# Optimization experiments

Hardware: AMD Instinct MI355X
Metric: run time of the kernel (lower is better)

The kernel has to match this reference:

```python
import jax, jax.numpy as jnp
import numpy as np

B, T, HID = 2, 2048, 1024
NH, HD = 16, 64          # attn_heads, head_size (NH*HD == HID)
FF = 4 * HID
LN_EPS = 1e-5            # torch nn.LayerNorm default


def setup_inputs() -> dict:
    key = jax.random.key(0)
    ks = jax.random.split(key, 14)
    s = lambda fan_in: fan_in ** -0.5
    return {
        "embedding": jax.random.normal(ks[0], (B, T, HID), jnp.float32),
        # per-head q/k/v projections stacked: [HID, NH, HD] (no bias, as in torch code)
        "Wq": jax.random.normal(ks[1], (HID, NH, HD), jnp.float32) * s(HID),
        "Wk": jax.random.normal(ks[2], (HID, NH, HD), jnp.float32) * s(HID),
        "Wv": jax.random.normal(ks[3], (HID, NH, HD), jnp.float32) * s(HID),
        "Wo": jax.random.normal(ks[4], (HID, HID), jnp.float32) * s(HID),
        "W1": jax.random.normal(ks[5], (HID, FF), jnp.float32) * s(HID),
        "b1": jnp.zeros((FF,), jnp.float32),
        "W2": jax.random.normal(ks[6], (FF, HID), jnp.float32) * s(FF),
        "b2": jnp.zeros((HID,), jnp.float32),
        "g1": jnp.ones((HID,), jnp.float32),
        "be1": jnp.zeros((HID,), jnp.float32),
        "g2": jnp.ones((HID,), jnp.float32),
        "be2": jnp.zeros((HID,), jnp.float32),
    }


def _layer_norm(h, g, b):
    mu = jnp.mean(h, axis=-1, keepdims=True)
    var = jnp.mean(jnp.square(h - mu), axis=-1, keepdims=True)
    return (h - mu) * jax.lax.rsqrt(var + LN_EPS) * g + b


def _block(x, Wq, Wk, Wv, Wo, W1, b1, W2, b2, g1, be1, g2, be2):
    # --- causal multi-head self-attention (pre-LN) ---
    h = _layer_norm(x, g1, be1)
    q = jnp.einsum('btd,dhk->bhtk', h, Wq)
    k = jnp.einsum('btd,dhk->bhtk', h, Wk)
    v = jnp.einsum('btd,dhk->bhtk', h, Wv)
    scores = jnp.einsum('bhtk,bhsk->bhts', q, k) * (HD ** -0.5)
    causal = jnp.tril(jnp.ones((T, T), bool))
    scores = jnp.where(causal, scores, -jnp.inf)
    attn = jax.nn.softmax(scores, axis=-1)
    ctx = jnp.einsum('bhts,bhsk->bhtk', attn, v)          # [B,NH,T,HD]
    ctx = ctx.transpose(0, 2, 1, 3).reshape(x.shape[0], x.shape[1], HID)
    x = x + ctx @ Wo
    # --- feed-forward (pre-LN) ---
    h2 = _layer_norm(x, g2, be2)
    ff = jax.nn.relu(h2 @ W1 + b1) @ W2 + b2
    return x + ff


def reference(embedding, Wq, Wk, Wv, Wo, W1, b1, W2, b2, g1, be1, g2, be2):
    return _block(embedding, Wq, Wk, Wv, Wo, W1, b1, W2, b2, g1, be1, g2, be2)
```

## Files before the change

kernel.cpp:

```cpp
#include <hip/hip_runtime.h>
#include <math.h>

#define HIDDEN 1024
#define SEQ    2048
#define NHEAD  16
#define HDIM   64
#define ROWS   (2 * SEQ)

typedef float  floatx4  __attribute__((ext_vector_type(4)));
typedef float  floatx16 __attribute__((ext_vector_type(16)));
typedef __bf16 bf16x8   __attribute__((ext_vector_type(8)));
typedef __bf16 bf16x4   __attribute__((ext_vector_type(4)));

#define AS1(p) ((const __attribute__((address_space(1))) void*)(p))
#define AS3(p) ((__attribute__((address_space(3))) void*)(p))

#define SWZ(row, chunk) ((((chunk) ^ ((row) & 7)) * 8))

__global__ __launch_bounds__(256) void prep_all(const float* __restrict__ Wq,
                                                const float* __restrict__ Wk,
                                                const float* __restrict__ Wv,
                                                const float* __restrict__ Wo,
                                                const float* __restrict__ W1,
                                                const float* __restrict__ W2,
                                                __bf16* __restrict__ BtQKV,
                                                __bf16* __restrict__ BtO,
                                                __bf16* __restrict__ Bt1,
                                                __bf16* __restrict__ Bt2,
                                                const float* __restrict__ emb,
                                                const float* __restrict__ g1,
                                                const float* __restrict__ be1,
                                                __bf16* __restrict__ h,
                                                float* __restrict__ xout) {
    int id = blockIdx.x;
    int tid = threadIdx.x;
    if (id >= 12288) {
        int row = id - 12288;
        size_t i = (size_t)row * HIDDEN + tid * 4;
        float4 v = *(const float4*)(emb + i);
        *(float4*)(xout + i) = v;
        float s  = v.x + v.y + v.z + v.w;
        float s2 = v.x * v.x + v.y * v.y + v.z * v.z + v.w * v.w;
#pragma unroll
        for (int off = 1; off < 64; off <<= 1) {
            s  += __shfl_xor(s, off, 64);
            s2 += __shfl_xor(s2, off, 64);
        }
        __shared__ float red[8];
        int wid = tid >> 6;
        if ((tid & 63) == 0) { red[wid] = s; red[wid + 4] = s2; }
        __syncthreads();
        s  = red[0] + red[1] + red[2] + red[3];
        s2 = red[4] + red[5] + red[6] + red[7];
        float mu  = s * (1.0f / HIDDEN);
        float var = fmaxf(s2 * (1.0f / HIDDEN) - mu * mu, 0.0f);
        float inv = rsqrtf(var + 1e-5f);
        float4 gv = *(const float4*)(g1 + tid * 4);
        float4 bv = *(const float4*)(be1 + tid * 4);
        bf16x4 o;
        o[0] = (__bf16)((v.x - mu) * inv * gv.x + bv.x);
        o[1] = (__bf16)((v.y - mu) * inv * gv.y + bv.y);
        o[2] = (__bf16)((v.z - mu) * inv * gv.z + bv.z);
        o[3] = (__bf16)((v.w - mu) * inv * gv.w + bv.w);
        *(bf16x4*)(h + i) = o;
        return;
    }
    __shared__ float t[32][33];
    const float* in; __bf16* out; int K, N, nt, kt;
    if (id < 4096) {
        int job = id >> 10, tt = id & 1023;
        nt = tt & 31; kt = tt >> 5; K = 1024; N = 1024;
        if (job == 0)      { in = Wq; out = BtQKV; }
        else if (job == 1) { in = Wk; out = BtQKV + 1024 * 1024; }
        else if (job == 2) { in = Wv; out = BtQKV + 2 * 1024 * 1024; }
        else               { in = Wo; out = BtO; }
    } else if (id < 8192) {
        int tt = id - 4096;
        nt = tt & 127; kt = tt >> 7; K = 1024; N = 4096; in = W1; out = Bt1;
    } else {
        int tt = id - 8192;
        nt = tt & 31; kt = tt >> 5; K = 4096; N = 1024; in = W2; out = Bt2;
    }
    int n0 = nt * 32, k0 = kt * 32;
    int r  = tid >> 3;
    int c4 = (tid & 7) * 4;
    float4 v = *(const float4*)(in + (size_t)(k0 + r) * N + n0 + c4);
    t[r][c4 + 0] = v.x; t[r][c4 + 1] = v.y; t[r][c4 + 2] = v.z; t[r][c4 + 3] = v.w;
    __syncthreads();
    bf16x4 o;
    o[0] = (__bf16)t[c4 + 0][r];
    o[1] = (__bf16)t[c4 + 1][r];
    o[2] = (__bf16)t[c4 + 2][r];
    o[3] = (__bf16)t[c4 + 3][r];
    int n = n0 + r, k = k0 + c4;
    size_t blk = (size_t)(n >> 5) * (K >> 4) + (k >> 4);
    int ln = ((k >> 3) & 1) * 32 + (n & 31);
    *(bf16x4*)(out + blk * 512 + ln * 8 + (k & 7)) = o;
}

__global__ __launch_bounds__(256) void red_ln(const float* __restrict__ b2,
                                              const float* __restrict__ g,
                                              const float* __restrict__ beta,
                                              float* __restrict__ out,
                                              __bf16* __restrict__ h2) {
    int row = blockIdx.x;
    int tid = threadIdx.x;
    size_t i = (size_t)row * HIDDEN + tid * 4;
    float4 v = *(const float4*)(out + i);
    float s  = v.x + v.y + v.z + v.w;
    float s2 = v.x * v.x + v.y * v.y + v.z * v.z + v.w * v.w;
#pragma unroll
    for (int off = 1; off < 64; off <<= 1) {
        s  += __shfl_xor(s, off, 64);
        s2 += __shfl_xor(s2, off, 64);
    }
    __shared__ float red[8];
    int wid = tid >> 6;
    if ((tid & 63) == 0) { red[wid] = s; red[wid + 4] = s2; }
    __syncthreads();
    s  = red[0] + red[1] + red[2] + red[3];
    s2 = red[4] + red[5] + red[6] + red[7];
    float mu  = s * (1.0f / HIDDEN);
    float var = fmaxf(s2 * (1.0f / HIDDEN) - mu * mu, 0.0f);
    float inv = rsqrtf(var + 1e-5f);
    float4 gv = *(const float4*)(g + tid * 4);
    float4 bv = *(const float4*)(beta + tid * 4);
    bf16x4 o;
    o[0] = (__bf16)((v.x - mu) * inv * gv.x + bv.x);
    o[1] = (__bf16)((v.y - mu) * inv * gv.y + bv.y);
    o[2] = (__bf16)((v.z - mu) * inv * gv.z + bv.z);
    o[3] = (__bf16)((v.w - mu) * inv * gv.w + bv.w);
    *(bf16x4*)(h2 + i) = o;
    float4 bb = *(const float4*)(b2 + tid * 4);
    v.x += bb.x; v.y += bb.y; v.z += bb.z; v.w += bb.w;
    *(float4*)(out + i) = v;
}

__device__ __forceinline__ void mfma_core128(const __bf16* __restrict__ A,
                                             const __bf16* __restrict__ BtF,
                                             int Kstride, int kbase, int Klen,
                                             int m0, int n0, int tid,
                                             floatx16 (&acc)[2][2]) {
    __shared__ __bf16 As[2 * 128 * 32];
    const int BUF = 128 * 32;
    int lane = tid & 63;
    int wave = tid >> 6;
    int wr = wave >> 1, wc = wave & 1;

    int sr = lane >> 2;
    int sk = 8 * ((lane & 3) ^ ((sr >> 1) & 3));
    const __bf16* ga0 = A + (size_t)(m0 + wave * 16 + sr) * Kstride + kbase + sk;
    const __bf16* ga1 = ga0 + (size_t)64 * Kstride;
    __bf16* la0 = &As[wave * 512];
    __bf16* la1 = &As[2048 + wave * 512];

    int fm = lane & 31;
    int gswz = (lane >> 1) & 3;
    int slot0 = ((lane >> 5) + 0) ^ gswz;
    int slot1 = ((lane >> 5) + 2) ^ gswz;

    const __bf16* bb = BtF + ((size_t)((n0 >> 5) + wc * 2) * (Kstride >> 4)) * 512
                     + (size_t)lane * 8;
    const size_t jstr = (size_t)(Kstride >> 4) * 512;
    int ci0 = kbase >> 4;

    __builtin_amdgcn_global_load_lds(AS1(ga0), AS3(la0), 16, 0, 0);
    __builtin_amdgcn_global_load_lds(AS1(ga1), AS3(la1), 16, 0, 0);
    bf16x8 bcur[2][2], bnxt[2][2];
#pragma unroll
    for (int j = 0; j < 2; j++)
#pragma unroll
        for (int t = 0; t < 2; t++)
            bcur[j][t] = *(const bf16x8*)(bb + j * jstr + (size_t)(ci0 + t) * 512);

    int buf = 0;
    for (int k0 = 0; k0 < Klen; k0 += 32, buf ^= 1) {
        __syncthreads();
        if (k0 + 32 < Klen) {
            int nb = (buf ^ 1) * BUF;
            __builtin_amdgcn_global_load_lds(AS1(ga0 + k0 + 32), AS3(la0 + nb), 16, 0, 0);
            __builtin_amdgcn_global_load_lds(AS1(ga1 + k0 + 32), AS3(la1 + nb), 16, 0, 0);
            int ci = ci0 + ((k0 + 32) >> 4);
#pragma unroll
            for (int j = 0; j < 2; j++)
#pragma unroll
                for (int t = 0; t < 2; t++)
                    bnxt[j][t] = *(const bf16x8*)(bb + j * jstr + (size_t)(ci + t) * 512);
        }
        const __bf16* Ab = As + buf * BUF;
        bf16x8 af[2][2];
#pragma unroll
        for (int i = 0; i < 2; i++) {
            const __bf16* rp = Ab + (size_t)(wr * 64 + i * 32 + fm) * 32;
            af[i][0] = *(const bf16x8*)(rp + slot0 * 8);
            af[i][1] = *(const bf16x8*)(rp + slot1 * 8);
        }
#pragma unroll
        for (int t = 0; t < 2; t++)
#pragma unroll
            for (int i = 0; i < 2; i++)
#pragma unroll
                for (int j = 0; j < 2; j++)
                    acc[i][j] = __builtin_amdgcn_mfma_f32_32x32x16_bf16(
                        af[i][t], bcur[j][t], acc[i][j], 0, 0, 0);
#pragma unroll
        for (int j = 0; j < 2; j++)
#pragma unroll
            for (int t = 0; t < 2; t++)
                bcur[j][t] = bnxt[j][t];
    }
}

template <typename OutT, bool BIAS, bool RELU>
__global__ __launch_bounds__(256) void mgemm(const __bf16* __restrict__ A,
                                             const __bf16* __restrict__ BtF,
                                             const float* __restrict__ bias,
                                             OutT* __restrict__ C,
                                             int N, int Kstride, int Klen) {
    int tid = threadIdx.x;
    int lane = tid & 63;
    int wave = tid >> 6;
    int m0 = blockIdx.x * 128, n0 = blockIdx.y * 128;
    int wr = wave >> 1, wc = wave & 1;
    floatx16 acc[2][2] = {};
    mfma_core128(A, BtF, Kstride, 0, Klen, m0, n0, tid, acc);

#pragma unroll
    for (int i = 0; i < 2; i++) {
#pragma unroll
        for (int j = 0; j < 2; j++) {
            int col  = n0 + wc * 64 + j * 32 + (lane & 31);
            int rowb = m0 + wr * 64 + i * 32 + 4 * (lane >> 5);
#pragma unroll
            for (int reg = 0; reg < 16; reg++) {
                int row = rowb + (reg & 3) + 8 * (reg >> 2);
                float v = acc[i][j][reg];
                if (BIAS) v += bias[col];
                if (RELU) v = fmaxf(v, 0.0f);
                C[(size_t)row * N + col] = (OutT)v;
            }
        }
    }
}

__global__ __launch_bounds__(256) void mgemm_qkv(const __bf16* __restrict__ A,
                                                 const __bf16* __restrict__ BtF,
                                                 __bf16* __restrict__ C,
                                                 __bf16* __restrict__ Vt) {
    const int N = 3072;
    int tid = threadIdx.x;
    int lane = tid & 63;
    int wave = tid >> 6;
    int m0 = blockIdx.x * 128, n0 = blockIdx.y * 128;
    int wr = wave >> 1, wc = wave & 1;
    floatx16 acc[2][2] = {};
    mfma_core128(A, BtF, 1024, 0, 1024, m0, n0, tid, acc);

#pragma unroll
    for (int i = 0; i < 2; i++) {
#pragma unroll
        for (int j = 0; j < 2; j++) {
            int col  = n0 + wc * 64 + j * 32 + (lane & 31);
            int rowb = m0 + wr * 64 + i * 32 + 4 * (lane >> 5);
            if (col < 2048) {
#pragma unroll
                for (int reg = 0; reg < 16; reg++) {
                    int row = rowb + (reg & 3) + 8 * (reg >> 2);
                    C[(size_t)row * N + col] = (__bf16)acc[i][j][reg];
                }
            } else {
                int vcol = col - 2048;
                int hh = vcol >> 6, dd = vcol & 63;
#pragma unroll
                for (int rq = 0; rq < 4; rq++) {
                    int row0 = rowb + 8 * rq;
                    int bb = row0 >> 11;
                    int tt = row0 & 2047;
                    bf16x4 pack;
                    pack[0] = (__bf16)acc[i][j][4 * rq + 0];
                    pack[1] = (__bf16)acc[i][j][4 * rq + 1];
                    pack[2] = (__bf16)acc[i][j][4 * rq + 2];
                    pack[3] = (__bf16)acc[i][j][4 * rq + 3];
                    *(bf16x4*)&Vt[(((size_t)bb * 16 + hh) * 64 + dd) * SEQ + tt] = pack;
                }
            }
        }
    }
}

__global__ __launch_bounds__(256) void mgemm_ska(const __bf16* __restrict__ A,
                                                 const __bf16* __restrict__ BtF,
                                                 float* __restrict__ out,
                                                 int N, int Kstride, int Klen) {
    int z = blockIdx.z;
    int tid = threadIdx.x;
    int lane = tid & 63;
    int wave = tid >> 6;
    int m0 = blockIdx.x * 128, n0 = blockIdx.y * 128;
    int wr = wave >> 1, wc = wave & 1;
    floatx16 acc[2][2] = {};
    mfma_core128(A, BtF, Kstride, z * Klen, Klen, m0, n0, tid, acc);

#pragma unroll
    for (int i = 0; i < 2; i++) {
#pragma unroll
        for (int j = 0; j < 2; j++) {
            int col  = n0 + wc * 64 + j * 32 + (lane & 31);
            int rowb = m0 + wr * 64 + i * 32 + 4 * (lane >> 5);
#pragma unroll
            for (int reg = 0; reg < 16; reg++) {
                int row = rowb + (reg & 3) + 8 * (reg >> 2);
                unsafeAtomicAdd(&out[(size_t)row * N + col], acc[i][j][reg]);
            }
        }
    }
}

__global__ __launch_bounds__(256) void attn_mfma(const __bf16* __restrict__ qkv,
                                                 const __bf16* __restrict__ Vt,
                                                 __bf16* __restrict__ ctx) {
    __shared__ __bf16 Ks[64 * 64];
    __shared__ __bf16 Vs[64 * 64];
    __shared__ __bf16 Ps[4][16 * 64];
    const int QKVW = 3 * HIDDEN;

    int bh = blockIdx.x;
    int qt = gridDim.y - 1 - blockIdx.y;
    int b = bh >> 4, h = bh & 15;
    int tid = threadIdx.x;
    int lane = tid & 63;
    int w = tid >> 6;
    int m = lane & 15;
    int g = lane >> 4;

    const float QSC = 1.44269504f / 8.0f;
    bf16x8 qf[2];
    {
        const __bf16* Qp = qkv + (size_t)(b * SEQ + qt * 64 + w * 16 + m) * QKVW
                         + h * HDIM + g * 8;
        qf[0] = *(const bf16x8*)(Qp);
        qf[1] = *(const bf16x8*)(Qp + 32);
#pragma unroll
        for (int t = 0; t < 2; t++)
#pragma unroll
            for (int i = 0; i < 8; i++)
                qf[t][i] = (__bf16)((float)qf[t][i] * QSC);
    }

    bf16x8 onesf;
#pragma unroll
    for (int i = 0; i < 8; i++) onesf[i] = (__bf16)1.0f;

    floatx4 oacc[4] = {};
    floatx4 lacc = {};

    int srow = tid >> 2;
    int sc0  = (tid & 3) * 2;
    const __bf16* Kg = qkv + (size_t)(b * SEQ) * QKVW + HIDDEN + h * HDIM;
    const __bf16* Vg = Vt + (size_t)bh * HDIM * SEQ;

    bf16x8 pk0, pk1, pv0, pv1;
    {
        const __bf16* kp = Kg + (size_t)srow * QKVW + sc0 * 8;
        pk0 = *(const bf16x8*)kp;
        pk1 = *(const bf16x8*)(kp + 8);
        const __bf16* vp = Vg + (size_t)srow * SEQ + sc0 * 8;
        pv0 = *(const bf16x8*)vp;
        pv1 = *(const bf16x8*)(vp + 8);
    }

    for (int kt = 0; kt <= qt; kt++) {
        __syncthreads();
        *(bf16x8*)&Ks[srow * 64 + SWZ(srow, sc0)]     = pk0;
        *(bf16x8*)&Ks[srow * 64 + SWZ(srow, sc0 + 1)] = pk1;
        *(bf16x8*)&Vs[srow * 64 + SWZ(srow, sc0)]     = pv0;
        *(bf16x8*)&Vs[srow * 64 + SWZ(srow, sc0 + 1)] = pv1;
        __syncthreads();

        if (kt < qt) {
            const __bf16* kp = Kg + (size_t)((kt + 1) * 64 + srow) * QKVW + sc0 * 8;
            pk0 = *(const bf16x8*)kp;
            pk1 = *(const bf16x8*)(kp + 8);
            const __bf16* vp = Vg + (size_t)srow * SEQ + (kt + 1) * 64 + sc0 * 8;
            pv0 = *(const bf16x8*)vp;
            pv1 = *(const bf16x8*)(vp + 8);
        }

        floatx4 sacc[4] = {};
#pragma unroll
        for (int j = 0; j < 4; j++) {
#pragma unroll
            for (int t = 0; t < 2; t++) {
                int kr = 16 * j + m;
                bf16x8 kf = *(const bf16x8*)&Ks[kr * 64 + SWZ(kr, g + 4 * t)];
                sacc[j] = __builtin_amdgcn_mfma_f32_16x16x32_bf16(
                    qf[t], kf, sacc[j], 0, 0, 0);
            }
        }

        if (kt == qt) {
            int qlocal = w * 16 + 4 * g;
#pragma unroll
            for (int j = 0; j < 4; j++)
#pragma unroll
                for (int r = 0; r < 4; r++)
                    if (16 * j + m > qlocal + r) sacc[j][r] = -INFINITY;
        }

        __bf16* Pw = &Ps[w][0];
#pragma unroll
        for (int j = 0; j < 4; j++)
#pragma unroll
            for (int r = 0; r < 4; r++) {
                float p = exp2f(sacc[j][r]);
                int row = 4 * g + r;
                int key = 16 * j + m;
                Pw[row * 64 + SWZ(row, key >> 3) + (key & 7)] = (__bf16)p;
            }

#pragma unroll
        for (int t = 0; t < 2; t++) {
            bf16x8 pf = *(const bf16x8*)&Pw[m * 64 + SWZ(m, g + 4 * t)];
            lacc = __builtin_amdgcn_mfma_f32_16x16x32_bf16(pf, onesf, lacc, 0, 0, 0);
#pragma unroll
            for (int jd = 0; jd < 4; jd++) {
                int vr = 16 * jd + m;
                bf16x8 vf = *(const bf16x8*)&Vs[vr * 64 + SWZ(vr, g + 4 * t)];
                oacc[jd] = __builtin_amdgcn_mfma_f32_16x16x32_bf16(
                    pf, vf, oacc[jd], 0, 0, 0);
            }
        }
    }

#pragma unroll
    for (int r = 0; r < 4; r++) {
        float invl = 1.0f / lacc[r];
        int row = qt * 64 + w * 16 + 4 * g + r;
        __bf16* cp = ctx + (size_t)(b * SEQ + row) * HIDDEN + h * HDIM;
#pragma unroll
        for (int jd = 0; jd < 4; jd++)
            cp[16 * jd + m] = (__bf16)(oacc[jd][r] * invl);
    }
}

extern "C" void kernel_launch(void* const* d_in, const int* in_sizes, int n_in,
                              void* d_out, int out_size, void* d_ws, size_t ws_size,
                              hipStream_t stream) {
    (void)in_sizes; (void)n_in; (void)out_size; (void)ws_size;
    const float* emb = (const float*)d_in[0];
    const float* Wq  = (const float*)d_in[1];
    const float* Wk  = (const float*)d_in[2];
    const float* Wv  = (const float*)d_in[3];
    const float* Wo  = (const float*)d_in[4];
    const float* W1  = (const float*)d_in[5];
    const float* b1  = (const float*)d_in[6];
    const float* W2  = (const float*)d_in[7];
    const float* b2  = (const float*)d_in[8];
    const float* g1  = (const float*)d_in[9];
    const float* be1 = (const float*)d_in[10];
    const float* g2  = (const float*)d_in[11];
    const float* be2 = (const float*)d_in[12];
    float* out = (float*)d_out;

    __bf16* wsb = (__bf16*)d_ws;
    const size_t ME = 1024 * 1024;
    __bf16* h     = wsb;
    __bf16* qkv   = wsb + 4 * ME;
    __bf16* ctx   = wsb;
    __bf16* ff1   = wsb;
    __bf16* h2    = wsb + 16 * ME;
    __bf16* BtQKV = wsb + 20 * ME;
    __bf16* BtO   = wsb + 23 * ME;
    __bf16* Bt1   = wsb + 24 * ME;
    __bf16* Bt2   = wsb + 28 * ME;
    __bf16* Vt    = wsb + 32 * ME;

    prep_all<<<16384, 256, 0, stream>>>(Wq, Wk, Wv, Wo, W1, W2,
                                        BtQKV, BtO, Bt1, Bt2,
                                        emb, g1, be1, h, out);

    mgemm_qkv<<<dim3(32, 24), 256, 0, stream>>>(h, BtQKV, qkv, Vt);

    attn_mfma<<<dim3(32, 32), 256, 0, stream>>>(qkv, Vt, ctx);

    mgemm_ska<<<dim3(32, 8, 2), 256, 0, stream>>>(
        ctx, BtO, out, 1024, 1024, 512);

    red_ln<<<ROWS, 256, 0, stream>>>(b2, g2, be2, out, h2);

    mgemm<__bf16, true, true><<<dim3(32, 32), 256, 0, stream>>>(
        h2, Bt1, b1, ff1, 4096, 1024, 1024);

    mgemm_ska<<<dim3(32, 8, 4), 256, 0, stream>>>(
        ff1, Bt2, out, 1024, 4096, 1024);
}
```

Before: 369.4 us.

## Replace split-K atomic accumulation with bf16 partial buffers and fused reductions

The split-K GEMMs for Wo and W2 now write per-split partial results as bf16 into workspace buffers instead of doing fp32 atomic adds into the output. Dedicated reduction kernels then sum the partials: one adds the embedding residual and applies the second LayerNorm, the other adds the FF partials, the bias and the residual. This removes atomic traffic and the embedding copy in prep, but adds an extra launch, extra partial-buffer reads and writes, and bf16 rounding of the partial sums.

```diff
diff --git a/kernel.cpp b/kernel.cpp
--- a/kernel.cpp
+++ b/kernel.cpp
@@ -30,15 +30,13 @@
                                                 const float* __restrict__ emb,
                                                 const float* __restrict__ g1,
                                                 const float* __restrict__ be1,
-                                                __bf16* __restrict__ h,
-                                                float* __restrict__ xout) {
+                                                __bf16* __restrict__ h) {
     int id = blockIdx.x;
     int tid = threadIdx.x;
     if (id >= 12288) {
         int row = id - 12288;
         size_t i = (size_t)row * HIDDEN + tid * 4;
         float4 v = *(const float4*)(emb + i);
-        *(float4*)(xout + i) = v;
         float s  = v.x + v.y + v.z + v.w;
         float s2 = v.x * v.x + v.y * v.y + v.z * v.z + v.w * v.w;
 #pragma unroll
@@ -98,15 +96,26 @@
     *(bf16x4*)(out + blk * 512 + ln * 8 + (k & 7)) = o;
 }
 
-__global__ __launch_bounds__(256) void red_ln(const float* __restrict__ b2,
-                                              const float* __restrict__ g,
-                                              const float* __restrict__ beta,
-                                              float* __restrict__ out,
-                                              __bf16* __restrict__ h2) {
+__global__ __launch_bounds__(256) void red_wo_ln(const float* __restrict__ emb,
+                                                 const __bf16* __restrict__ p0,
+                                                 const __bf16* __restrict__ p1,
+                                                 const float* __restrict__ g,
+                                                 const float* __restrict__ beta,
+                                                 float* __restrict__ out,
+                                                 __bf16* __restrict__ h2) {
     int row = blockIdx.x;
     int tid = threadIdx.x;
     size_t i = (size_t)row * HIDDEN + tid * 4;
-    float4 v = *(const float4*)(out + i);
+    float4 e = *(const float4*)(emb + i);
+    bf16x4 a = *(const bf16x4*)(p0 + i);
+    bf16x4 b = *(const bf16x4*)(p1 + i);
+    float4 v;
+    v.x = e.x + (float)a[0] + (float)b[0];
+    v.y = e.y + (float)a[1] + (float)b[1];
+    v.z = e.z + (float)a[2] + (float)b[2];
+    v.w = e.w + (float)a[3] + (float)b[3];
+    *(float4*)(out + i) = v;
+
     float s  = v.x + v.y + v.z + v.w;
     float s2 = v.x * v.x + v.y * v.y + v.z * v.z + v.w * v.w;
 #pragma unroll
@@ -131,9 +140,34 @@
     o[2] = (__bf16)((v.z - mu) * inv * gv.z + bv.z);
     o[3] = (__bf16)((v.w - mu) * inv * gv.w + bv.w);
     *(bf16x4*)(h2 + i) = o;
-    float4 bb = *(const float4*)(b2 + tid * 4);
-    v.x += bb.x; v.y += bb.y; v.z += bb.z; v.w += bb.w;
-    *(float4*)(out + i) = v;
+}
+
+__global__ __launch_bounds__(256) void red_w2(const __bf16* __restrict__ p0,
+                                              const __bf16* __restrict__ p3,
+                                              const float* __restrict__ b2,
+                                              float* __restrict__ out,
+                                              int N) {
+    size_t i = ((size_t)blockIdx.x * 256 + threadIdx.x) * 8;
+    const size_t MN = (size_t)ROWS * HIDDEN;
+    bf16x8 a = *(const bf16x8*)(p0 + i);
+    bf16x8 b = *(const bf16x8*)(p0 + MN + i);
+    bf16x8 c = *(const bf16x8*)(p0 + 2 * MN + i);
+    bf16x8 d = *(const bf16x8*)(p3 + i);
+    int col = (int)(i & (size_t)(N - 1));
+    float4 bb0 = *(const float4*)(b2 + col);
+    float4 bb1 = *(const float4*)(b2 + col + 4);
+    float4 o0 = *(const float4*)(out + i);
+    float4 o1 = *(const float4*)(out + i + 4);
+    o0.x += (float)a[0] + (float)b[0] + (float)c[0] + (float)d[0] + bb0.x;
+    o0.y += (float)a[1] + (float)b[1] + (float)c[1] + (float)d[1] + bb0.y;
+    o0.z += (float)a[2] + (float)b[2] + (float)c[2] + (float)d[2] + bb0.z;
+    o0.w += (float)a[3] + (float)b[3] + (float)c[3] + (float)d[3] + bb0.w;
+    o1.x += (float)a[4] + (float)b[4] + (float)c[4] + (float)d[4] + bb1.x;
+    o1.y += (float)a[5] + (float)b[5] + (float)c[5] + (float)d[5] + bb1.y;
+    o1.z += (float)a[6] + (float)b[6] + (float)c[6] + (float)d[6] + bb1.z;
+    o1.w += (float)a[7] + (float)b[7] + (float)c[7] + (float)d[7] + bb1.w;
+    *(float4*)(out + i)     = o0;
+    *(float4*)(out + i + 4) = o1;
 }
 
 __device__ __forceinline__ void mfma_core128(const __bf16* __restrict__ A,
@@ -288,11 +322,13 @@
     }
 }
 
-__global__ __launch_bounds__(256) void mgemm_ska(const __bf16* __restrict__ A,
-                                                 const __bf16* __restrict__ BtF,
-                                                 float* __restrict__ out,
-                                                 int N, int Kstride, int Klen) {
+__global__ __launch_bounds__(256) void mgemm_sk(const __bf16* __restrict__ A,
+                                                const __bf16* __restrict__ BtF,
+                                                __bf16* __restrict__ P0,
+                                                __bf16* __restrict__ P3,
+                                                int M, int N, int Kstride, int Klen) {
     int z = blockIdx.z;
+    __bf16* C = (z == 3) ? P3 : (P0 + (size_t)z * M * N);
     int tid = threadIdx.x;
     int lane = tid & 63;
     int wave = tid >> 6;
@@ -310,7 +346,7 @@
 #pragma unroll
             for (int reg = 0; reg < 16; reg++) {
                 int row = rowb + (reg & 3) + 8 * (reg >> 2);
-                unsafeAtomicAdd(&out[(size_t)row * N + col], acc[i][j][reg]);
+                C[(size_t)row * N + col] = (__bf16)acc[i][j][reg];
             }
         }
     }
@@ -474,23 +510,26 @@
     __bf16* Bt1   = wsb + 24 * ME;
     __bf16* Bt2   = wsb + 28 * ME;
     __bf16* Vt    = wsb + 32 * ME;
+    __bf16* woP   = wsb + 4 * ME;
+    __bf16* w2P0  = wsb + 16 * ME;
+    __bf16* w2P3  = wsb + 32 * ME;
 
     prep_all<<<16384, 256, 0, stream>>>(Wq, Wk, Wv, Wo, W1, W2,
                                         BtQKV, BtO, Bt1, Bt2,
-                                        emb, g1, be1, h, out);
+                                        emb, g1, be1, h);
 
     mgemm_qkv<<<dim3(32, 24), 256, 0, stream>>>(h, BtQKV, qkv, Vt);
 
     attn_mfma<<<dim3(32, 32), 256, 0, stream>>>(qkv, Vt, ctx);
 
-    mgemm_ska<<<dim3(32, 8, 2), 256, 0, stream>>>(
-        ctx, BtO, out, 1024, 1024, 512);
-
-    red_ln<<<ROWS, 256, 0, stream>>>(b2, g2, be2, out, h2);
+    mgemm_sk<<<dim3(32, 8, 2), 256, 0, stream>>>(
+        ctx, BtO, woP, nullptr, ROWS, 1024, 1024, 512);
+    red_wo_ln<<<ROWS, 256, 0, stream>>>(emb, woP, woP + 4 * ME, g2, be2, out, h2);
 
     mgemm<__bf16, true, true><<<dim3(32, 32), 256, 0, stream>>>(
         h2, Bt1, b1, ff1, 4096, 1024, 1024);
 
-    mgemm_ska<<<dim3(32, 8, 4), 256, 0, stream>>>(
-        ff1, Bt2, out, 1024, 4096, 1024);
-}
+    mgemm_sk<<<dim3(32, 8, 4), 256, 0, stream>>>(
+        ff1, Bt2, w2P0, w2P3, ROWS, 1024, 4096, 1024);
+    red_w2<<<2048, 256, 0, stream>>>(w2P0, w2P3, b2, out, 1024);
+}
```

Result: faster. 322.6 us (-12.7%).
